# Kernel tuning notes

Hardware: AMD Instinct MI355X
Metric: run time of the kernel (lower is better)

Reference implementation:

```python
import jax, jax.numpy as jnp
import numpy as np

N_HEAD = 16

def setup_inputs() -> dict:
    key = jax.random.key(0)
    ks = jax.random.split(key, 5)
    B, T, C = 2, 2048, 1024
    s = 1.0 / np.sqrt(C)
    return {
        "x": jax.random.normal(ks[0], (B, T, C), dtype=jnp.float32),
        "Wq": jax.random.normal(ks[1], (C, C), dtype=jnp.float32) * s,
        "Wk": jax.random.normal(ks[2], (C, C), dtype=jnp.float32) * s,
        "Wv": jax.random.normal(ks[3], (C, C), dtype=jnp.float32) * s,
        "Wo": jax.random.normal(ks[4], (C, C), dtype=jnp.float32) * s,
        "bo": jnp.zeros((C,), dtype=jnp.float32),
    }

def reference(x, Wq, Wk, Wv, Wo, bo):
    B, T, C = x.shape
    H = N_HEAD
    D = C // H

    def shape(t):  # (B,T,C) -> (B,H,T,D)
        return t.reshape(B, T, H, D).transpose(0, 2, 1, 3)

    q = shape(x @ Wq)
    k = shape(x @ Wk)
    v = shape(x @ Wv)

    # scores: (B,H,T,Tk), Tk == T (no past_kv)
    att = jnp.einsum("bhtd,bhsd->bhts", q, k) * (1.0 / np.sqrt(D))
    i = jnp.arange(T)[:, None]
    j = jnp.arange(T)[None, :]
    causal = (j <= i)  # (T, Tk)
    att = jnp.where(causal[None, None], att, -jnp.inf)
    att = jax.nn.softmax(att, axis=-1)  # dropout=0.0 -> identity

    out = jnp.einsum("bhts,bhsd->bhtd", att, v)
    out = out.transpose(0, 2, 1, 3).reshape(B, T, C)
    out = out @ Wo + bo
    return out, (k, v)
```

## Files before the change

### kernel.cpp

```cpp
#include <hip/hip_runtime.h>
#include <hip/hip_bf16.h>

constexpr int B_ = 2;
constexpr int T_ = 2048;
constexpr int C_ = 1024;
constexpr int H_ = 16;
constexpr int D_ = 64;
constexpr int M_ = B_ * T_;

typedef __attribute__((ext_vector_type(8))) short bf16x8;
typedef __attribute__((ext_vector_type(4))) float f32x4;
typedef const __attribute__((address_space(1))) void gaddr_t;
typedef __attribute__((address_space(3))) void laddr_t;

__device__ __forceinline__ unsigned short f2bf(float f) {
    unsigned u = __float_as_uint(f);
    return (unsigned short)((u + 0x7fffu + ((u >> 16) & 1u)) >> 16);
}

union BF8 { bf16x8 v; __hip_bfloat162 h[4]; };

__device__ __forceinline__ bf16x8 cvt8(const float4 a, const float4 b) {
    BF8 r;
    r.h[0] = __float22bfloat162_rn(make_float2(a.x, a.y));
    r.h[1] = __float22bfloat162_rn(make_float2(a.z, a.w));
    r.h[2] = __float22bfloat162_rn(make_float2(b.x, b.y));
    r.h[3] = __float22bfloat162_rn(make_float2(b.z, b.w));
    return r.v;
}

__global__ __launch_bounds__(256)
void cast_x(const float* __restrict__ x, unsigned short* __restrict__ xb, int n4)
{
    for (int i = blockIdx.x * 256 + threadIdx.x; i < n4; i += gridDim.x * 256) {
        float4 v = ((const float4*)x)[i];
        union { __hip_bfloat162 h[2]; ushort4 u; } o;
        o.h[0] = __float22bfloat162_rn(make_float2(v.x, v.y));
        o.h[1] = __float22bfloat162_rn(make_float2(v.z, v.w));
        ((ushort4*)xb)[i] = o.u;
    }
}

__global__ __launch_bounds__(256)
void tcast_w(const float* __restrict__ Wq, const float* __restrict__ Wk,
             const float* __restrict__ Wv, const float* __restrict__ Wo,
             unsigned short* __restrict__ wtb)
{
    __shared__ float tile[64][65];
    const int z = blockIdx.z;
    const float* W = (z == 0) ? Wq : (z == 1) ? Wk : (z == 2) ? Wv : Wo;
    unsigned short* O = wtb + (size_t)z * C_ * C_;

    const int tid = threadIdx.x;
    const int n0 = blockIdx.x * 64, k0 = blockIdx.y * 64;
    const int r = tid >> 4, c4 = (tid & 15) * 4;

#pragma unroll
    for (int i = 0; i < 4; ++i) {
        const int kk = i * 16 + r;
        float4 v = *(const float4*)(W + (size_t)(k0 + kk) * C_ + n0 + c4);
        tile[c4 + 0][kk] = v.x;
        tile[c4 + 1][kk] = v.y;
        tile[c4 + 2][kk] = v.z;
        tile[c4 + 3][kk] = v.w;
    }
    __syncthreads();
#pragma unroll
    for (int i = 0; i < 4; ++i) {
        const int nn = i * 16 + r;
        ushort4 o;
        o.x = f2bf(tile[nn][c4 + 0]);
        o.y = f2bf(tile[nn][c4 + 1]);
        o.z = f2bf(tile[nn][c4 + 2]);
        o.w = f2bf(tile[nn][c4 + 3]);
        *(ushort4*)(O + (size_t)(n0 + nn) * C_ + k0 + c4) = o;
    }
}

template<int WRITE_KB>
__global__ __launch_bounds__(256)
void gemm_qkv(const unsigned short* __restrict__ xb, const unsigned short* __restrict__ wtb,
              unsigned short* __restrict__ qb, float* __restrict__ kout,
              float* __restrict__ vout, unsigned short* __restrict__ kb)
{
    __shared__ unsigned short As[128 * 64];
    __shared__ unsigned short Bs[128 * 64];

    const int tid = threadIdx.x;
    const int which = blockIdx.x >> 3;
    const int n0 = (blockIdx.x & 7) * 128;
    const int m0 = blockIdx.y * 128;
    const unsigned short* wt = wtb + (size_t)which * C_ * C_;

    const int lane = tid & 63, w = tid >> 6;
    const int wm = (w >> 1) * 64, wn = (w & 1) * 64;
    const int fr = lane & 15, qd = lane >> 4;

    f32x4 acc[4][4] = {};

    for (int k0 = 0; k0 < C_; k0 += 64) {
#pragma unroll
        for (int cc = 0; cc < 4; ++cc) {
            const int c = tid + cc * 256;
            const int row = c >> 3, dg = (c & 7) ^ (row & 7);
            __builtin_amdgcn_global_load_lds(
                (gaddr_t*)(xb + (size_t)(m0 + row) * C_ + k0 + dg * 8),
                (laddr_t*)((char*)As + (size_t)c * 16), 16, 0, 0);
        }
#pragma unroll
        for (int cc = 0; cc < 4; ++cc) {
            const int c = tid + cc * 256;
            const int row = c >> 3, dg = (c & 7) ^ (row & 7);
            __builtin_amdgcn_global_load_lds(
                (gaddr_t*)(wt + (size_t)(n0 + row) * C_ + k0 + dg * 8),
                (laddr_t*)((char*)Bs + (size_t)c * 16), 16, 0, 0);
        }
        __syncthreads();

#pragma unroll
        for (int half = 0; half < 2; ++half) {
            bf16x8 af[4], bfv[4];
#pragma unroll
            for (int mt = 0; mt < 4; ++mt) {
                const int row = wm + mt * 16 + fr, dg = half * 4 + qd;
                af[mt] = *(const bf16x8*)&As[row * 64 + ((dg ^ (row & 7)) * 8)];
            }
#pragma unroll
            for (int nt = 0; nt < 4; ++nt) {
                const int row = wn + nt * 16 + fr, dg = half * 4 + qd;
                bfv[nt] = *(const bf16x8*)&Bs[row * 64 + ((dg ^ (row & 7)) * 8)];
            }
#pragma unroll
            for (int mt = 0; mt < 4; ++mt)
#pragma unroll
                for (int nt = 0; nt < 4; ++nt)
                    acc[mt][nt] = __builtin_amdgcn_mfma_f32_16x16x32_bf16(
                        af[mt], bfv[nt], acc[mt][nt], 0, 0, 0);
        }
        __syncthreads();
    }

#pragma unroll
    for (int mt = 0; mt < 4; ++mt) {
#pragma unroll
        for (int nt = 0; nt < 4; ++nt) {
            const int ncol = n0 + wn + nt * 16 + fr;
            const int h = ncol >> 6, d = ncol & 63;
#pragma unroll
            for (int r = 0; r < 4; ++r) {
                const int mm = m0 + wm + mt * 16 + qd * 4 + r;
                const int b = mm >> 11, t = mm & (T_ - 1);
                const int bh = b * H_ + h;
                const size_t off = ((size_t)bh * T_ + t) * D_ + d;
                const float val = acc[mt][nt][r];
                if (which == 0)      qb[off]   = f2bf(val);
                else if (which == 1) {
                    kout[off] = val;
                    if (WRITE_KB) kb[off] = f2bf(val);
                } else               vout[off] = val;
            }
        }
    }
}

__global__ __launch_bounds__(256)
void transpose_v(const float* __restrict__ v, unsigned short* __restrict__ vtt)
{
    __shared__ unsigned short tile[64 * 66];
    const int tid = threadIdx.x;
    const int bh = blockIdx.y, t0 = blockIdx.x * 64;
    const float* vB = v + ((size_t)bh * T_ + t0) * D_;

    const int r = tid >> 4, c4 = (tid & 15) * 4;
#pragma unroll
    for (int i = 0; i < 4; ++i) {
        const int tt = i * 16 + r;
        float4 x4 = *(const float4*)(vB + tt * D_ + c4);
        tile[(c4 + 0) * 66 + tt] = f2bf(x4.x);
        tile[(c4 + 1) * 66 + tt] = f2bf(x4.y);
        tile[(c4 + 2) * 66 + tt] = f2bf(x4.z);
        tile[(c4 + 3) * 66 + tt] = f2bf(x4.w);
    }
    __syncthreads();
    unsigned short* out = vtt + (((size_t)bh * (T_ / 64) + (t0 >> 6)) * 64) * 64;
#pragma unroll
    for (int i = 0; i < 4; ++i) {
        const int d = i * 16 + r;
        ushort4 o;
        o.x = tile[d * 66 + c4 + 0];
        o.y = tile[d * 66 + c4 + 1];
        o.z = tile[d * 66 + c4 + 2];
        o.w = tile[d * 66 + c4 + 3];
        *(ushort4*)(out + d * 64 + c4) = o;
    }
}

__global__ __launch_bounds__(256)
void gemm_o(const unsigned short* __restrict__ ab, const unsigned short* __restrict__ wot,
            const float* __restrict__ bo, float* __restrict__ out)
{
    __shared__ unsigned short As[128 * 64];
    __shared__ unsigned short Bs[128 * 64];

    const int tid = threadIdx.x;
    const int n0 = blockIdx.x * 128;
    const int m0 = blockIdx.y * 128;

    const int lane = tid & 63, w = tid >> 6;
    const int wm = (w >> 1) * 64, wn = (w & 1) * 64;
    const int fr = lane & 15, qd = lane >> 4;

    f32x4 acc[4][4] = {};

    for (int k0 = 0; k0 < C_; k0 += 64) {
#pragma unroll
        for (int cc = 0; cc < 4; ++cc) {
            const int c = tid + cc * 256;
            const int row = c >> 3, dg = (c & 7) ^ (row & 7);
            __builtin_amdgcn_global_load_lds(
                (gaddr_t*)(ab + (size_t)(m0 + row) * C_ + k0 + dg * 8),
                (laddr_t*)((char*)As + (size_t)c * 16), 16, 0, 0);
        }
#pragma unroll
        for (int cc = 0; cc < 4; ++cc) {
            const int c = tid + cc * 256;
            const int row = c >> 3, dg = (c & 7) ^ (row & 7);
            __builtin_amdgcn_global_load_lds(
                (gaddr_t*)(wot + (size_t)(n0 + row) * C_ + k0 + dg * 8),
                (laddr_t*)((char*)Bs + (size_t)c * 16), 16, 0, 0);
        }
        __syncthreads();

#pragma unroll
        for (int half = 0; half < 2; ++half) {
            bf16x8 af[4], bfv[4];
#pragma unroll
            for (int mt = 0; mt < 4; ++mt) {
                const int row = wm + mt * 16 + fr, dg = half * 4 + qd;
                af[mt] = *(const bf16x8*)&As[row * 64 + ((dg ^ (row & 7)) * 8)];
            }
#pragma unroll
            for (int nt = 0; nt < 4; ++nt) {
                const int row = wn + nt * 16 + fr, dg = half * 4 + qd;
                bfv[nt] = *(const bf16x8*)&Bs[row * 64 + ((dg ^ (row & 7)) * 8)];
            }
#pragma unroll
            for (int mt = 0; mt < 4; ++mt)
#pragma unroll
                for (int nt = 0; nt < 4; ++nt)
                    acc[mt][nt] = __builtin_amdgcn_mfma_f32_16x16x32_bf16(
                        af[mt], bfv[nt], acc[mt][nt], 0, 0, 0);
        }
        __syncthreads();
    }

#pragma unroll
    for (int mt = 0; mt < 4; ++mt) {
#pragma unroll
        for (int nt = 0; nt < 4; ++nt) {
            const int ncol = n0 + wn + nt * 16 + fr;
            const float bb = bo[ncol];
#pragma unroll
            for (int r = 0; r < 4; ++r) {
                const int mm = m0 + wm + mt * 16 + qd * 4 + r;
                out[(size_t)mm * C_ + ncol] = acc[mt][nt][r] + bb;
            }
        }
    }
}

__global__ __launch_bounds__(256)
void attn_lds(const unsigned short* __restrict__ qb, const unsigned short* __restrict__ kb,
              const unsigned short* __restrict__ vtt, unsigned short* __restrict__ attb)
{
    __shared__ unsigned short Ks[64 * 64];
    __shared__ unsigned short Vs[64 * 64];
    __shared__ alignas(16) unsigned short Pt[4][16 * 72];

    const int tid = threadIdx.x;
    const int lane = tid & 63, w = tid >> 6;
    const int fr = lane & 15, qd = lane >> 4;

    const int blk = blockIdx.x;
    const int xcd = blk & 7, within = blk >> 3;
    const int bh = xcd * 4 + (within & 3);
    const int jj = within >> 2;
    const int kk_ = jj >> 3, ii_ = jj & 7;
    const int qt = (kk_ == 0) ? (31 - ii_) : (kk_ == 1) ? ii_
                 : (kk_ == 2) ? (23 - ii_) : (8 + ii_);
    const int b = bh >> 4, h = bh & 15;

    unsigned short* Pw = Pt[w];
    const unsigned short* qB = qb  + (size_t)bh * T_ * D_;
    const unsigned short* kB = kb  + (size_t)bh * T_ * D_;
    const unsigned short* vT = vtt + (size_t)bh * (T_ / 64) * 64 * 64;

    const int qr0 = qt * 64 + w * 16;
    const int qrow_g = qr0 + fr;

    bf16x8 aq0 = *(const bf16x8*)(qB + (size_t)(qr0 + fr) * D_ + qd * 8);
    bf16x8 aq1 = *(const bf16x8*)(qB + (size_t)(qr0 + fr) * D_ + 32 + qd * 8);

    f32x4 accT[4] = {};
    float l_i = 0.0f;
    const float sc2 = 0.18033688f;

    const int L0 = w * 128 + lane, L1 = L0 + 64;
    const int r0 = L0 >> 3, e0 = (((L0 & 7) ^ (r0 & 7)) * 8);
    const int r1 = L1 >> 3, e1 = (((L1 & 7) ^ (r1 & 7)) * 8);
    laddr_t* dK0 = (laddr_t*)((char*)Ks + (size_t)L0 * 16);
    laddr_t* dK1 = (laddr_t*)((char*)Ks + (size_t)L1 * 16);
    laddr_t* dV0 = (laddr_t*)((char*)Vs + (size_t)L0 * 16);
    laddr_t* dV1 = (laddr_t*)((char*)Vs + (size_t)L1 * 16);

    for (int jt = 0; jt <= qt; ++jt) {
        __syncthreads();
        {
            const unsigned short* kt = kB + (size_t)(jt * 64) * 64;
            const unsigned short* vt = vT + (size_t)jt * 4096;
            __builtin_amdgcn_global_load_lds((gaddr_t*)(kt + r0 * 64 + e0), dK0, 16, 0, 0);
            __builtin_amdgcn_global_load_lds((gaddr_t*)(kt + r1 * 64 + e1), dK1, 16, 0, 0);
            __builtin_amdgcn_global_load_lds((gaddr_t*)(vt + r0 * 64 + e0), dV0, 16, 0, 0);
            __builtin_amdgcn_global_load_lds((gaddr_t*)(vt + r1 * 64 + e1), dV1, 16, 0, 0);
        }
        __syncthreads();

        bf16x8 bk[8];
#pragma unroll
        for (int q8 = 0; q8 < 8; ++q8) {
            const int row = (q8 >> 1) * 16 + fr;
            const int dg = (q8 & 1) * 4 + qd;
            bk[q8] = *(const bf16x8*)&Ks[row * 64 + ((dg ^ (row & 7)) * 8)];
        }

        f32x4 s4[4] = {};
#pragma unroll
        for (int nt = 0; nt < 4; ++nt) {
            s4[nt] = __builtin_amdgcn_mfma_f32_16x16x32_bf16(bk[nt * 2 + 0], aq0, s4[nt], 0, 0, 0);
            s4[nt] = __builtin_amdgcn_mfma_f32_16x16x32_bf16(bk[nt * 2 + 1], aq1, s4[nt], 0, 0, 0);
        }

        if (jt == qt) {
            const int kbase = jt * 64 + qd * 4;
#pragma unroll
            for (int nt = 0; nt < 4; ++nt)
#pragma unroll
            for (int r = 0; r < 4; ++r) {
                const int kcol = kbase + nt * 16 + r;
                const float pv = (kcol <= qrow_g)
                               ? __builtin_amdgcn_exp2f(s4[nt][r] * sc2) : 0.0f;
                s4[nt][r] = pv;
                l_i += pv;
            }
        } else {
#pragma unroll
            for (int nt = 0; nt < 4; ++nt)
#pragma unroll
            for (int r = 0; r < 4; ++r) {
                const float pv = __builtin_amdgcn_exp2f(s4[nt][r] * sc2);
                s4[nt][r] = pv;
                l_i += pv;
            }
        }

#pragma unroll
        for (int nt = 0; nt < 4; ++nt) {
            union { __hip_bfloat162 h2[2]; unsigned long long u; } pk;
            pk.h2[0] = __float22bfloat162_rn(make_float2(s4[nt][0], s4[nt][1]));
            pk.h2[1] = __float22bfloat162_rn(make_float2(s4[nt][2], s4[nt][3]));
            *(unsigned long long*)&Pw[fr * 72 + nt * 16 + qd * 4] = pk.u;
        }
        const bf16x8 ap0 = *(const bf16x8*)&Pw[fr * 72 + qd * 8];
        const bf16x8 ap1 = *(const bf16x8*)&Pw[fr * 72 + 32 + qd * 8];

        bf16x8 bv[8];
#pragma unroll
        for (int q8 = 0; q8 < 8; ++q8) {
            const int row = (q8 >> 1) * 16 + fr;
            const int dg = (q8 & 1) * 4 + qd;
            bv[q8] = *(const bf16x8*)&Vs[row * 64 + ((dg ^ (row & 7)) * 8)];
        }

#pragma unroll
        for (int nt = 0; nt < 4; ++nt) {
            accT[nt] = __builtin_amdgcn_mfma_f32_16x16x32_bf16(bv[nt * 2 + 0], ap0, accT[nt], 0, 0, 0);
            accT[nt] = __builtin_amdgcn_mfma_f32_16x16x32_bf16(bv[nt * 2 + 1], ap1, accT[nt], 0, 0, 0);
        }
    }

    l_i += __shfl_xor(l_i, 16);
    l_i += __shfl_xor(l_i, 32);
    const float inv = 1.0f / l_i;

#pragma unroll
    for (int nt = 0; nt < 4; ++nt) {
        union { __hip_bfloat162 h2[2]; unsigned long long u; } ok;
        ok.h2[0] = __float22bfloat162_rn(make_float2(accT[nt][0] * inv, accT[nt][1] * inv));
        ok.h2[1] = __float22bfloat162_rn(make_float2(accT[nt][2] * inv, accT[nt][3] * inv));
        *(unsigned long long*)&Pw[fr * 72 + nt * 16 + qd * 4] = ok.u;
    }
    {
        const int row = lane >> 2, d0 = (lane & 3) * 16;
        const bf16x8 o0 = *(const bf16x8*)&Pw[row * 72 + d0];
        const bf16x8 o1 = *(const bf16x8*)&Pw[row * 72 + d0 + 8];
        unsigned short* op = attb + ((size_t)b * T_ + qr0 + row) * C_ + h * 64 + d0;
        *(bf16x8*)op = o0;
        *(bf16x8*)(op + 8) = o1;
    }
}

__global__ __launch_bounds__(256)
void attn_v4(const unsigned short* __restrict__ qb, const float* __restrict__ kf,
             const unsigned short* __restrict__ vtt, unsigned short* __restrict__ attb)
{
    __shared__ alignas(16) unsigned short Pt[4][16 * 72];

    const int tid = threadIdx.x;
    const int lane = tid & 63, w = tid >> 6;
    const int fr = lane & 15, qd = lane >> 4;

    const int blk = blockIdx.x;
    const int xcd = blk & 7, within = blk >> 3;
    const int bh = xcd * 4 + (within & 3);
    const int jj = within >> 2;
    const int kk_ = jj >> 3, ii_ = jj & 7;
    const int qt = (kk_ == 0) ? (31 - ii_) : (kk_ == 1) ? ii_
                 : (kk_ == 2) ? (23 - ii_) : (8 + ii_);
    const int b = bh >> 4, h = bh & 15;

    unsigned short* Pw = Pt[w];
    const unsigned short* qB = qb  + (size_t)bh * T_ * D_;
    const float*          kB = kf  + (size_t)bh * T_ * D_;
    const unsigned short* vT = vtt + (size_t)bh * (T_ / 64) * 64 * 64;

    const int qr0 = qt * 64 + w * 16;
    const int qrow_g = qr0 + fr;

    bf16x8 aq0 = *(const bf16x8*)(qB + (size_t)(qr0 + fr) * D_ + qd * 8);
    bf16x8 aq1 = *(const bf16x8*)(qB + (size_t)(qr0 + fr) * D_ + 32 + qd * 8);

    f32x4 accT[4] = {};
    float l_i = 0.0f;
    const float sc2 = 0.18033688f;

    for (int jt = 0; jt <= qt; ++jt) {
        bf16x8 bk[8];
#pragma unroll
        for (int q8 = 0; q8 < 8; ++q8) {
            const float* p = kB + (size_t)(jt * 64 + (q8 >> 1) * 16 + fr) * D_
                           + (q8 & 1) * 32 + qd * 8;
            bk[q8] = cvt8(*(const float4*)p, *(const float4*)(p + 4));
        }
        f32x4 s4[4] = {};
#pragma unroll
        for (int nt = 0; nt < 4; ++nt) {
            s4[nt] = __builtin_amdgcn_mfma_f32_16x16x32_bf16(bk[nt * 2 + 0], aq0, s4[nt], 0, 0, 0);
            s4[nt] = __builtin_amdgcn_mfma_f32_16x16x32_bf16(bk[nt * 2 + 1], aq1, s4[nt], 0, 0, 0);
        }
        if (jt == qt) {
            const int kbase = jt * 64 + qd * 4;
#pragma unroll
            for (int nt = 0; nt < 4; ++nt)
#pragma unroll
            for (int r = 0; r < 4; ++r) {
                const int kcol = kbase + nt * 16 + r;
                const float pv = (kcol <= qrow_g)
                               ? __builtin_amdgcn_exp2f(s4[nt][r] * sc2) : 0.0f;
                s4[nt][r] = pv; l_i += pv;
            }
        } else {
#pragma unroll
            for (int nt = 0; nt < 4; ++nt)
#pragma unroll
            for (int r = 0; r < 4; ++r) {
                const float pv = __builtin_amdgcn_exp2f(s4[nt][r] * sc2);
                s4[nt][r] = pv; l_i += pv;
            }
        }
#pragma unroll
        for (int nt = 0; nt < 4; ++nt) {
            union { __hip_bfloat162 h2[2]; unsigned long long u; } pk;
            pk.h2[0] = __float22bfloat162_rn(make_float2(s4[nt][0], s4[nt][1]));
            pk.h2[1] = __float22bfloat162_rn(make_float2(s4[nt][2], s4[nt][3]));
            *(unsigned long long*)&Pw[fr * 72 + nt * 16 + qd * 4] = pk.u;
        }
        const bf16x8 ap0 = *(const bf16x8*)&Pw[fr * 72 + qd * 8];
        const bf16x8 ap1 = *(const bf16x8*)&Pw[fr * 72 + 32 + qd * 8];

        bf16x8 bv[8];
#pragma unroll
        for (int q8 = 0; q8 < 8; ++q8)
            bv[q8] = *(const bf16x8*)(vT + (size_t)jt * 4096
                                      + ((q8 >> 1) * 16 + fr) * 64 + (q8 & 1) * 32 + qd * 8);
#pragma unroll
        for (int nt = 0; nt < 4; ++nt) {
            accT[nt] = __builtin_amdgcn_mfma_f32_16x16x32_bf16(bv[nt * 2 + 0], ap0, accT[nt], 0, 0, 0);
            accT[nt] = __builtin_amdgcn_mfma_f32_16x16x32_bf16(bv[nt * 2 + 1], ap1, accT[nt], 0, 0, 0);
        }
    }

    l_i += __shfl_xor(l_i, 16);
    l_i += __shfl_xor(l_i, 32);
    const float inv = 1.0f / l_i;
#pragma unroll
    for (int nt = 0; nt < 4; ++nt) {
        union { __hip_bfloat162 h2[2]; unsigned long long u; } ok;
        ok.h2[0] = __float22bfloat162_rn(make_float2(accT[nt][0] * inv, accT[nt][1] * inv));
        ok.h2[1] = __float22bfloat162_rn(make_float2(accT[nt][2] * inv, accT[nt][3] * inv));
        *(unsigned long long*)&Pw[fr * 72 + nt * 16 + qd * 4] = ok.u;
    }
    {
        const int row = lane >> 2, d0 = (lane & 3) * 16;
        const bf16x8 o0 = *(const bf16x8*)&Pw[row * 72 + d0];
        const bf16x8 o1 = *(const bf16x8*)&Pw[row * 72 + d0 + 8];
        unsigned short* op = attb + ((size_t)b * T_ + qr0 + row) * C_ + h * 64 + d0;
        *(bf16x8*)op = o0;
        *(bf16x8*)(op + 8) = o1;
    }
}

extern "C" void kernel_launch(void* const* d_in, const int* in_sizes, int n_in,
                              void* d_out, int out_size, void* d_ws, size_t ws_size,
                              hipStream_t stream)
{
    (void)in_sizes; (void)n_in; (void)out_size;
    const float* x  = (const float*)d_in[0];
    const float* Wq = (const float*)d_in[1];
    const float* Wk = (const float*)d_in[2];
    const float* Wv = (const float*)d_in[3];
    const float* Wo = (const float*)d_in[4];
    const float* bo = (const float*)d_in[5];

    float* out  = (float*)d_out;
    float* kout = out  + (size_t)M_ * C_;
    float* vout = kout + (size_t)B_ * H_ * T_ * D_;

    unsigned short* xb   = (unsigned short*)d_ws;
    unsigned short* wtb  = xb  + (size_t)M_ * C_;
    unsigned short* qb   = wtb + (size_t)4 * C_ * C_;
    unsigned short* vtt  = qb  + (size_t)M_ * C_;
    unsigned short* kb   = vtt + (size_t)M_ * C_;
    unsigned short* attb = xb;
    const bool use_kb = ws_size >= (size_t)40 * 1024 * 1024;

    cast_x<<<1024, 256, 0, stream>>>(x, xb, (M_ * C_) / 4);
    tcast_w<<<dim3(16, 16, 4), 256, 0, stream>>>(Wq, Wk, Wv, Wo, wtb);

    if (use_kb)
        gemm_qkv<1><<<dim3(24, M_ / 128), 256, 0, stream>>>(xb, wtb, qb, kout, vout, kb);
    else
        gemm_qkv<0><<<dim3(24, M_ / 128), 256, 0, stream>>>(xb, wtb, qb, kout, vout, kb);

    transpose_v<<<dim3(T_ / 64, B_ * H_), 256, 0, stream>>>(vout, vtt);

    if (use_kb)
        attn_lds<<<1024, 256, 0, stream>>>(qb, kb, vtt, attb);
    else
        attn_v4<<<1024, 256, 0, stream>>>(qb, kout, vtt, attb);

    gemm_o<<<dim3(8, M_ / 128), 256, 0, stream>>>(attb, wtb + (size_t)3 * C_ * C_, bo, out);
}
```

Measured before the change: 202.6 us.

## Fuse V transpose into QKV GEMM, vectorize epilogues, double-buffer attention K/V

Swaps the MFMA operand order so each lane holds four consecutive output columns, which lets the QKV and output GEMM epilogues use vector stores. The bf16 transposed-V write moves into the QKV GEMM epilogue, removing the separate transpose_v kernel launch and its re-read of V. The attention kernel now double-buffers K/V tiles in LDS, prefetching the next tile while computing the current one, and raises wave priority around the MFMA blocks. The transposed-V writes are scattered 2-byte stores, and the doubled LDS use may lower occupancy.

New measurement: 202.7 us. About the same (+0.0%).

```diff
diff --git a/kernel.cpp b/kernel.cpp
--- a/kernel.cpp
+++ b/kernel.cpp
@@ -81,7 +81,8 @@
 __global__ __launch_bounds__(256)
 void gemm_qkv(const unsigned short* __restrict__ xb, const unsigned short* __restrict__ wtb,
               unsigned short* __restrict__ qb, float* __restrict__ kout,
-              float* __restrict__ vout, unsigned short* __restrict__ kb)
+              float* __restrict__ vout, unsigned short* __restrict__ kb,
+              unsigned short* __restrict__ vtt)
 {
     __shared__ unsigned short As[128 * 64];
     __shared__ unsigned short Bs[128 * 64];
@@ -135,63 +136,38 @@
 #pragma unroll
                 for (int nt = 0; nt < 4; ++nt)
                     acc[mt][nt] = __builtin_amdgcn_mfma_f32_16x16x32_bf16(
-                        af[mt], bfv[nt], acc[mt][nt], 0, 0, 0);
+                        bfv[nt], af[mt], acc[mt][nt], 0, 0, 0);
         }
         __syncthreads();
     }
 
 #pragma unroll
     for (int mt = 0; mt < 4; ++mt) {
-#pragma unroll
-        for (int nt = 0; nt < 4; ++nt) {
-            const int ncol = n0 + wn + nt * 16 + fr;
-            const int h = ncol >> 6, d = ncol & 63;
-#pragma unroll
-            for (int r = 0; r < 4; ++r) {
-                const int mm = m0 + wm + mt * 16 + qd * 4 + r;
-                const int b = mm >> 11, t = mm & (T_ - 1);
-                const int bh = b * H_ + h;
-                const size_t off = ((size_t)bh * T_ + t) * D_ + d;
-                const float val = acc[mt][nt][r];
-                if (which == 0)      qb[off]   = f2bf(val);
-                else if (which == 1) {
-                    kout[off] = val;
-                    if (WRITE_KB) kb[off] = f2bf(val);
-                } else               vout[off] = val;
-            }
-        }
-    }
-}
-
-__global__ __launch_bounds__(256)
-void transpose_v(const float* __restrict__ v, unsigned short* __restrict__ vtt)
-{
-    __shared__ unsigned short tile[64 * 66];
-    const int tid = threadIdx.x;
-    const int bh = blockIdx.y, t0 = blockIdx.x * 64;
-    const float* vB = v + ((size_t)bh * T_ + t0) * D_;
-
-    const int r = tid >> 4, c4 = (tid & 15) * 4;
-#pragma unroll
-    for (int i = 0; i < 4; ++i) {
-        const int tt = i * 16 + r;
-        float4 x4 = *(const float4*)(vB + tt * D_ + c4);
-        tile[(c4 + 0) * 66 + tt] = f2bf(x4.x);
-        tile[(c4 + 1) * 66 + tt] = f2bf(x4.y);
-        tile[(c4 + 2) * 66 + tt] = f2bf(x4.z);
-        tile[(c4 + 3) * 66 + tt] = f2bf(x4.w);
-    }
-    __syncthreads();
-    unsigned short* out = vtt + (((size_t)bh * (T_ / 64) + (t0 >> 6)) * 64) * 64;
-#pragma unroll
-    for (int i = 0; i < 4; ++i) {
-        const int d = i * 16 + r;
-        ushort4 o;
-        o.x = tile[d * 66 + c4 + 0];
-        o.y = tile[d * 66 + c4 + 1];
-        o.z = tile[d * 66 + c4 + 2];
-        o.w = tile[d * 66 + c4 + 3];
-        *(ushort4*)(out + d * 64 + c4) = o;
+        const int mm = m0 + wm + mt * 16 + fr;
+        const int b = mm >> 11, t = mm & (T_ - 1);
+#pragma unroll
+        for (int nt = 0; nt < 4; ++nt) {
+            const int nn = n0 + wn + nt * 16 + qd * 4;
+            const int h = nn >> 6, d0 = nn & 63;
+            const int bh = b * H_ + h;
+            const size_t off = ((size_t)bh * T_ + t) * D_ + d0;
+            const f32x4 a4 = acc[mt][nt];
+            if (which == 0) {
+                *(ushort4*)(qb + off) =
+                    make_ushort4(f2bf(a4[0]), f2bf(a4[1]), f2bf(a4[2]), f2bf(a4[3]));
+            } else if (which == 1) {
+                *(float4*)(kout + off) = make_float4(a4[0], a4[1], a4[2], a4[3]);
+                if (WRITE_KB)
+                    *(ushort4*)(kb + off) =
+                        make_ushort4(f2bf(a4[0]), f2bf(a4[1]), f2bf(a4[2]), f2bf(a4[3]));
+            } else {
+                *(float4*)(vout + off) = make_float4(a4[0], a4[1], a4[2], a4[3]);
+                unsigned short* vb = vtt
+                    + (((size_t)bh * (T_ / 64) + (t >> 6)) * 64 + d0) * 64 + (t & 63);
+#pragma unroll
+                for (int r = 0; r < 4; ++r) vb[(size_t)r * 64] = f2bf(a4[r]);
+            }
+        }
     }
 }
 
@@ -249,22 +225,21 @@
 #pragma unroll
                 for (int nt = 0; nt < 4; ++nt)
                     acc[mt][nt] = __builtin_amdgcn_mfma_f32_16x16x32_bf16(
-                        af[mt], bfv[nt], acc[mt][nt], 0, 0, 0);
+                        bfv[nt], af[mt], acc[mt][nt], 0, 0, 0);
         }
         __syncthreads();
     }
 
 #pragma unroll
     for (int mt = 0; mt < 4; ++mt) {
-#pragma unroll
-        for (int nt = 0; nt < 4; ++nt) {
-            const int ncol = n0 + wn + nt * 16 + fr;
-            const float bb = bo[ncol];
-#pragma unroll
-            for (int r = 0; r < 4; ++r) {
-                const int mm = m0 + wm + mt * 16 + qd * 4 + r;
-                out[(size_t)mm * C_ + ncol] = acc[mt][nt][r] + bb;
-            }
+        const int mm = m0 + wm + mt * 16 + fr;
+#pragma unroll
+        for (int nt = 0; nt < 4; ++nt) {
+            const int nn = n0 + wn + nt * 16 + qd * 4;
+            const float4 b4 = *(const float4*)(bo + nn);
+            *(float4*)(out + (size_t)mm * C_ + nn) =
+                make_float4(acc[mt][nt][0] + b4.x, acc[mt][nt][1] + b4.y,
+                            acc[mt][nt][2] + b4.z, acc[mt][nt][3] + b4.w);
         }
     }
 }
@@ -273,8 +248,8 @@
 void attn_lds(const unsigned short* __restrict__ qb, const unsigned short* __restrict__ kb,
               const unsigned short* __restrict__ vtt, unsigned short* __restrict__ attb)
 {
-    __shared__ unsigned short Ks[64 * 64];
-    __shared__ unsigned short Vs[64 * 64];
+    __shared__ unsigned short Ks[2][64 * 64];
+    __shared__ unsigned short Vs[2][64 * 64];
     __shared__ alignas(16) unsigned short Pt[4][16 * 72];
 
     const int tid = threadIdx.x;
@@ -308,37 +283,56 @@
     const int L0 = w * 128 + lane, L1 = L0 + 64;
     const int r0 = L0 >> 3, e0 = (((L0 & 7) ^ (r0 & 7)) * 8);
     const int r1 = L1 >> 3, e1 = (((L1 & 7) ^ (r1 & 7)) * 8);
-    laddr_t* dK0 = (laddr_t*)((char*)Ks + (size_t)L0 * 16);
-    laddr_t* dK1 = (laddr_t*)((char*)Ks + (size_t)L1 * 16);
-    laddr_t* dV0 = (laddr_t*)((char*)Vs + (size_t)L0 * 16);
-    laddr_t* dV1 = (laddr_t*)((char*)Vs + (size_t)L1 * 16);
+
+    {
+        __builtin_amdgcn_global_load_lds((gaddr_t*)(kB + r0 * 64 + e0),
+            (laddr_t*)((char*)Ks[0] + (size_t)L0 * 16), 16, 0, 0);
+        __builtin_amdgcn_global_load_lds((gaddr_t*)(kB + r1 * 64 + e1),
+            (laddr_t*)((char*)Ks[0] + (size_t)L1 * 16), 16, 0, 0);
+        __builtin_amdgcn_global_load_lds((gaddr_t*)(vT + r0 * 64 + e0),
+            (laddr_t*)((char*)Vs[0] + (size_t)L0 * 16), 16, 0, 0);
+        __builtin_amdgcn_global_load_lds((gaddr_t*)(vT + r1 * 64 + e1),
+            (laddr_t*)((char*)Vs[0] + (size_t)L1 * 16), 16, 0, 0);
+    }
+    asm volatile("s_waitcnt vmcnt(0)" ::: "memory");
+    __builtin_amdgcn_s_barrier();
+    __builtin_amdgcn_sched_barrier(0);
 
     for (int jt = 0; jt <= qt; ++jt) {
-        __syncthreads();
-        {
-            const unsigned short* kt = kB + (size_t)(jt * 64) * 64;
-            const unsigned short* vt = vT + (size_t)jt * 4096;
-            __builtin_amdgcn_global_load_lds((gaddr_t*)(kt + r0 * 64 + e0), dK0, 16, 0, 0);
-            __builtin_amdgcn_global_load_lds((gaddr_t*)(kt + r1 * 64 + e1), dK1, 16, 0, 0);
-            __builtin_amdgcn_global_load_lds((gaddr_t*)(vt + r0 * 64 + e0), dV0, 16, 0, 0);
-            __builtin_amdgcn_global_load_lds((gaddr_t*)(vt + r1 * 64 + e1), dV1, 16, 0, 0);
-        }
-        __syncthreads();
+        const int cur = jt & 1;
+        if (jt < qt) {
+            const unsigned short* kt = kB + (size_t)((jt + 1) * 64) * 64;
+            const unsigned short* vt = vT + (size_t)(jt + 1) * 4096;
+            char* Kn = (char*)Ks[cur ^ 1];
+            char* Vn = (char*)Vs[cur ^ 1];
+            __builtin_amdgcn_global_load_lds((gaddr_t*)(kt + r0 * 64 + e0),
+                (laddr_t*)(Kn + (size_t)L0 * 16), 16, 0, 0);
+            __builtin_amdgcn_global_load_lds((gaddr_t*)(kt + r1 * 64 + e1),
+                (laddr_t*)(Kn + (size_t)L1 * 16), 16, 0, 0);
+            __builtin_amdgcn_global_load_lds((gaddr_t*)(vt + r0 * 64 + e0),
+                (laddr_t*)(Vn + (size_t)L0 * 16), 16, 0, 0);
+            __builtin_amdgcn_global_load_lds((gaddr_t*)(vt + r1 * 64 + e1),
+                (laddr_t*)(Vn + (size_t)L1 * 16), 16, 0, 0);
+        }
+        const unsigned short* Kc = Ks[cur];
+        const unsigned short* Vc = Vs[cur];
 
         bf16x8 bk[8];
 #pragma unroll
         for (int q8 = 0; q8 < 8; ++q8) {
             const int row = (q8 >> 1) * 16 + fr;
             const int dg = (q8 & 1) * 4 + qd;
-            bk[q8] = *(const bf16x8*)&Ks[row * 64 + ((dg ^ (row & 7)) * 8)];
+            bk[q8] = *(const bf16x8*)&Kc[row * 64 + ((dg ^ (row & 7)) * 8)];
         }
 
         f32x4 s4[4] = {};
+        __builtin_amdgcn_s_setprio(1);
 #pragma unroll
         for (int nt = 0; nt < 4; ++nt) {
             s4[nt] = __builtin_amdgcn_mfma_f32_16x16x32_bf16(bk[nt * 2 + 0], aq0, s4[nt], 0, 0, 0);
             s4[nt] = __builtin_amdgcn_mfma_f32_16x16x32_bf16(bk[nt * 2 + 1], aq1, s4[nt], 0, 0, 0);
         }
+        __builtin_amdgcn_s_setprio(0);
 
         if (jt == qt) {
             const int kbase = jt * 64 + qd * 4;
@@ -378,14 +372,20 @@
         for (int q8 = 0; q8 < 8; ++q8) {
             const int row = (q8 >> 1) * 16 + fr;
             const int dg = (q8 & 1) * 4 + qd;
-            bv[q8] = *(const bf16x8*)&Vs[row * 64 + ((dg ^ (row & 7)) * 8)];
-        }
-
+            bv[q8] = *(const bf16x8*)&Vc[row * 64 + ((dg ^ (row & 7)) * 8)];
+        }
+
+        __builtin_amdgcn_s_setprio(1);
 #pragma unroll
         for (int nt = 0; nt < 4; ++nt) {
             accT[nt] = __builtin_amdgcn_mfma_f32_16x16x32_bf16(bv[nt * 2 + 0], ap0, accT[nt], 0, 0, 0);
             accT[nt] = __builtin_amdgcn_mfma_f32_16x16x32_bf16(bv[nt * 2 + 1], ap1, accT[nt], 0, 0, 0);
         }
+        __builtin_amdgcn_s_setprio(0);
+
+        asm volatile("s_waitcnt vmcnt(0)" ::: "memory");
+        __builtin_amdgcn_s_barrier();
+        __builtin_amdgcn_sched_barrier(0);
     }
 
     l_i += __shfl_xor(l_i, 16);
@@ -547,11 +547,9 @@
     tcast_w<<<dim3(16, 16, 4), 256, 0, stream>>>(Wq, Wk, Wv, Wo, wtb);
 
     if (use_kb)
-        gemm_qkv<1><<<dim3(24, M_ / 128), 256, 0, stream>>>(xb, wtb, qb, kout, vout, kb);
+        gemm_qkv<1><<<dim3(24, M_ / 128), 256, 0, stream>>>(xb, wtb, qb, kout, vout, kb, vtt);
     else
-        gemm_qkv<0><<<dim3(24, M_ / 128), 256, 0, stream>>>(xb, wtb, qb, kout, vout, kb);
-
-    transpose_v<<<dim3(T_ / 64, B_ * H_), 256, 0, stream>>>(vout, vtt);
+        gemm_qkv<0><<<dim3(24, M_ / 128), 256, 0, stream>>>(xb, wtb, qb, kout, vout, kb, vtt);
 
     if (use_kb)
         attn_lds<<<1024, 256, 0, stream>>>(qb, kb, vtt, attb);
```
